# Kernel optimization log

Measured on AMD Instinct MI355X. Metric: run time of the kernel, lower is better.

## Reference

```python
import jax, jax.numpy as jnp
import numpy as np

N, E, F, H, D, O = 100000, 1600000, 128, 128, 64, 1


def setup_inputs() -> dict:
    key = jax.random.key(0)
    ks = jax.random.split(key, 10)
    s = lambda f: np.float32(1.0 / np.sqrt(f))
    return {
        "x": jax.random.normal(ks[0], (N, F), jnp.float32),
        "edge_index": jax.random.randint(ks[1], (2, E), 0, N),
        "W1": jax.random.normal(ks[2], (F, H), jnp.float32) * s(F),
        "b1": jnp.zeros((H,), jnp.float32),
        "Wh": jax.random.normal(ks[3], (H, H), jnp.float32) * s(H),
        "bh": jnp.zeros((H,), jnp.float32),
        "W2": jax.random.normal(ks[4], (H, D), jnp.float32) * s(H),
        "b2": jnp.zeros((D,), jnp.float32),
        "Wo": jax.random.normal(ks[5], (D, O), jnp.float32) * s(D),
        "bo": jnp.zeros((O,), jnp.float32),
    }


def _gcn_layer(h, W, b, src, dst, norm, n):
    # linear transform then normalized sparse aggregation (GCNConv)
    h = h @ W                                   # [n, out]
    msg = h[src] * norm[:, None]                # gather + scale, [E+n, out]
    return jax.ops.segment_sum(msg, dst, num_segments=n) + b


def reference(x, edge_index, W1, b1, Wh, bh, W2, b2, Wo, bo):
    n = x.shape[0]
    loop = jnp.arange(n, dtype=edge_index.dtype)
    src = jnp.concatenate([edge_index[0], loop])  # add self loops
    dst = jnp.concatenate([edge_index[1], loop])
    deg = jax.ops.segment_sum(jnp.ones_like(dst, dtype=x.dtype), dst, num_segments=n)
    dinv = jnp.where(deg > 0, jax.lax.rsqrt(deg), 0.0)
    norm = dinv[src] * dinv[dst]                  # sym-normalized edge weights

    h = jax.nn.relu(_gcn_layer(x, W1, b1, src, dst, norm, n))
    h = jax.nn.relu(_gcn_layer(h, Wh, bh, src, dst, norm, n))
    z = _gcn_layer(h, W2, b2, src, dst, norm, n)  # embedding (no relu after gcn2)
    return z @ Wo + bo                            # node_classification logits [n, 1]
```

## Files before the change

### kernel.cpp

```cpp
#include <hip/hip_runtime.h>
#include <hip/hip_fp16.h>


#define CHUNK 8192
#define ASTR 136

using f16x8 = __attribute__((ext_vector_type(8))) _Float16;
using f32x4 = __attribute__((ext_vector_type(4))) float;

__global__ __launch_bounds__(256) void histH(const int* __restrict__ dst, int* __restrict__ hist,
                                             int E, int NBKT, int NB) {
    __shared__ int bins[1024];
    int blk = blockIdx.x;
    for (int i = threadIdx.x; i < NBKT; i += 256) bins[i] = 0;
    __syncthreads();
    int beg = blk * CHUNK, end = min(E, beg + CHUNK);
    for (int e = beg + threadIdx.x; e < end; e += 256)
        atomicAdd(&bins[dst[e] >> 7], 1);
    __syncthreads();
    for (int i = threadIdx.x; i < NBKT; i += 256)
        hist[i * NB + blk] = bins[i];
}

__global__ __launch_bounds__(256) void scanA(int* __restrict__ hist, int* __restrict__ binsum,
                                             int NBKT, int NB) {
    int wave = (int)((blockIdx.x * (size_t)blockDim.x + threadIdx.x) >> 6);
    if (wave >= NBKT) return;
    int lane = threadIdx.x & 63;
    int* row = hist + (size_t)wave * NB;
    int running = 0;
    for (int b0 = 0; b0 < NB; b0 += 64) {
        int idx = b0 + lane;
        int v = (idx < NB) ? row[idx] : 0;
        int s = v;
#pragma unroll
        for (int off = 1; off < 64; off <<= 1) {
            int u = __shfl_up(s, off, 64);
            if (lane >= off) s += u;
        }
        if (idx < NB) row[idx] = running + s - v;
        running += __shfl(s, 63, 64);
    }
    if (lane == 0) binsum[wave] = running;
}

__global__ void scanK2(const int* __restrict__ binsum, int* __restrict__ binbase,
                       int NBKT, int E) {
    __shared__ int s[1024];
    int t = threadIdx.x;
    int v = (t < NBKT) ? binsum[t] : 0;
    s[t] = v;
    __syncthreads();
    for (int off = 1; off < 1024; off <<= 1) {
        int u = (t >= off) ? s[t - off] : 0;
        __syncthreads();
        s[t] += u;
        __syncthreads();
    }
    if (t < NBKT) binbase[t] = s[t] - v;
    if (t == 0) binbase[NBKT] = E;
}

__global__ __launch_bounds__(256) void scatterH(const int* __restrict__ src,
                                                const int* __restrict__ dst,
                                                const int* __restrict__ hist,
                                                const int* __restrict__ binbase,
                                                int* __restrict__ tmp,
                                                int E, int NBKT, int NB) {
    __shared__ int offs[1024];
    int blk = blockIdx.x;
    for (int i = threadIdx.x; i < NBKT; i += 256)
        offs[i] = hist[i * NB + blk] + binbase[i];
    __syncthreads();
    int beg = blk * CHUNK, end = min(E, beg + CHUNK);
    for (int e = beg + threadIdx.x; e < end; e += 256) {
        int d = dst[e];
        int pos = atomicAdd(&offs[d >> 7], 1);
        tmp[pos] = ((d & 127) << 17) | src[e];
    }
}

__global__ __launch_bounds__(256) void bucket_csr(const int* __restrict__ tmp,
                                                  const int* __restrict__ binbase,
                                                  int* __restrict__ rowptr,
                                                  int* __restrict__ srcidx,
                                                  float* __restrict__ dinv,
                                                  int n) {
    __shared__ int cnt[128], sc[128], cnt2[128];
    int b = blockIdx.x;
    int bstart = binbase[b], bend = binbase[b + 1];
    if (threadIdx.x < 128) cnt[threadIdx.x] = 0;
    __syncthreads();
    for (int e = bstart + threadIdx.x; e < bend; e += 256)
        atomicAdd(&cnt[tmp[e] >> 17], 1);
    __syncthreads();
    if (threadIdx.x < 128) sc[threadIdx.x] = cnt[threadIdx.x];
    __syncthreads();
    for (int off = 1; off < 128; off <<= 1) {
        int u = 0;
        if (threadIdx.x < 128 && threadIdx.x >= off) u = sc[threadIdx.x - off];
        __syncthreads();
        if (threadIdx.x < 128) sc[threadIdx.x] += u;
        __syncthreads();
    }
    if (threadIdx.x < 128) {
        int excl = sc[threadIdx.x] - cnt[threadIdx.x];
        cnt2[threadIdx.x] = excl;
        int id = b * 128 + threadIdx.x;
        if (id <= n) rowptr[id] = bstart + excl;
        if (id < n) dinv[id] = rsqrtf((float)cnt[threadIdx.x] + 1.0f);
    }
    __syncthreads();
    for (int e = bstart + threadIdx.x; e < bend; e += 256) {
        int p = tmp[e];
        int pos = bstart + atomicAdd(&cnt2[p >> 17], 1);
        srcidx[pos] = p & 0x1FFFF;
    }
}

__global__ __launch_bounds__(256) void prep_w(const float* __restrict__ W1,
                                              const float* __restrict__ Wh,
                                              const float* __restrict__ W2,
                                              const float* __restrict__ b2,
                                              const float* __restrict__ Wo,
                                              const float* __restrict__ bo,
                                              __half* __restrict__ Wt1,
                                              __half* __restrict__ WtH,
                                              float* __restrict__ w3,
                                              float* __restrict__ c3) {
    const float* W = blockIdx.x ? Wh : W1;
    __half* Wt = blockIdx.x ? WtH : Wt1;
    for (int i = threadIdx.x; i < 16384; i += 256) {
        int c = i >> 7, k = i & 127;
        Wt[c * 128 + k] = __float2half(W[k * 128 + c]);
    }
    if (blockIdx.x == 0 && threadIdx.x < 128) {
        int j = threadIdx.x;
        float s = 0.f;
        for (int d = 0; d < 64; ++d) s += W2[j * 64 + d] * Wo[d];
        w3[j] = s;
        if (j == 0) {
            float c = 0.f;
            for (int d = 0; d < 64; ++d) c += b2[d] * Wo[d];
            *c3 = c + bo[0];
        }
    }
}

template<typename AT>
__global__ __launch_bounds__(256) void gemm_mfma(const AT* __restrict__ A,
                                                 const __half* __restrict__ Wt,
                                                 const float* __restrict__ dinv,
                                                 __half* __restrict__ Ch, int n) {
    __shared__ _Float16 Al[64 * ASTR];
    __shared__ _Float16 Wl[128 * ASTR];
    const int tid = threadIdx.x;
    const int row0 = blockIdx.x * 64;

#pragma unroll
    for (int i = 0; i < 8; ++i) {
        int idx = tid + 256 * i;
        int c = idx >> 4, q = idx & 15;
        uint4 v = *(const uint4*)(Wt + c * 128 + q * 8);
        *(uint4*)(&Wl[c * ASTR + q * 8]) = v;
    }
#pragma unroll
    for (int i = 0; i < 4; ++i) {
        int idx = tid + 256 * i;
        int r = idx >> 4, q = idx & 15;
        int row = row0 + r;
        uint4 u;
        if constexpr (sizeof(AT) == 2) {
            u = (row < n) ? *(const uint4*)((const __half*)A + (size_t)row * 128 + q * 8)
                          : make_uint4(0u, 0u, 0u, 0u);
        } else {
            if (row < n) {
                const float* ap = (const float*)A + (size_t)row * 128 + q * 8;
                float4 v0 = *(const float4*)ap;
                float4 v1 = *(const float4*)(ap + 4);
                __half2 p0 = __floats2half2_rn(v0.x, v0.y);
                __half2 p1 = __floats2half2_rn(v0.z, v0.w);
                __half2 p2 = __floats2half2_rn(v1.x, v1.y);
                __half2 p3 = __floats2half2_rn(v1.z, v1.w);
                u.x = *(unsigned*)&p0; u.y = *(unsigned*)&p1;
                u.z = *(unsigned*)&p2; u.w = *(unsigned*)&p3;
            } else u = make_uint4(0u, 0u, 0u, 0u);
        }
        *(uint4*)(&Al[r * ASTR + q * 8]) = u;
    }
    __syncthreads();

    const int wave = tid >> 6, lane = tid & 63;
    const int wr = (wave >> 1) * 32;
    const int wc = (wave & 1) * 64;
    const int l = lane & 15, g = lane >> 4;

    f32x4 acc[2][4];
#pragma unroll
    for (int i = 0; i < 2; ++i)
#pragma unroll
        for (int j = 0; j < 4; ++j) acc[i][j] = (f32x4){0.f, 0.f, 0.f, 0.f};

#pragma unroll
    for (int kk = 0; kk < 128; kk += 32) {
        int ko = kk + g * 8;
        f16x8 a0 = *(const f16x8*)(&Al[(wr + l) * ASTR + ko]);
        f16x8 a1 = *(const f16x8*)(&Al[(wr + 16 + l) * ASTR + ko]);
        f16x8 b0 = *(const f16x8*)(&Wl[(wc + l) * ASTR + ko]);
        f16x8 b1 = *(const f16x8*)(&Wl[(wc + 16 + l) * ASTR + ko]);
        f16x8 b2 = *(const f16x8*)(&Wl[(wc + 32 + l) * ASTR + ko]);
        f16x8 b3 = *(const f16x8*)(&Wl[(wc + 48 + l) * ASTR + ko]);
        acc[0][0] = __builtin_amdgcn_mfma_f32_16x16x32_f16(a0, b0, acc[0][0], 0, 0, 0);
        acc[0][1] = __builtin_amdgcn_mfma_f32_16x16x32_f16(a0, b1, acc[0][1], 0, 0, 0);
        acc[0][2] = __builtin_amdgcn_mfma_f32_16x16x32_f16(a0, b2, acc[0][2], 0, 0, 0);
        acc[0][3] = __builtin_amdgcn_mfma_f32_16x16x32_f16(a0, b3, acc[0][3], 0, 0, 0);
        acc[1][0] = __builtin_amdgcn_mfma_f32_16x16x32_f16(a1, b0, acc[1][0], 0, 0, 0);
        acc[1][1] = __builtin_amdgcn_mfma_f32_16x16x32_f16(a1, b1, acc[1][1], 0, 0, 0);
        acc[1][2] = __builtin_amdgcn_mfma_f32_16x16x32_f16(a1, b2, acc[1][2], 0, 0, 0);
        acc[1][3] = __builtin_amdgcn_mfma_f32_16x16x32_f16(a1, b3, acc[1][3], 0, 0, 0);
    }

#pragma unroll
    for (int rt = 0; rt < 2; ++rt) {
#pragma unroll
        for (int j = 0; j < 4; ++j) {
            int row = row0 + wr + rt * 16 + g * 4 + j;
            if (row < n) {
                float di = dinv[row];
#pragma unroll
                for (int ct = 0; ct < 4; ++ct)
                    Ch[(size_t)row * 128 + wc + ct * 16 + l] =
                        __float2half(acc[rt][ct][j] * di);
            }
        }
    }
}

template<int MODE>
__global__ __launch_bounds__(256) void agg_csr(const int* __restrict__ rowptr,
                                               const int* __restrict__ srcidx,
                                               const float* __restrict__ dinv,
                                               const __half* __restrict__ Gh,
                                               const float* __restrict__ bias,
                                               const float* __restrict__ w3,
                                               void* __restrict__ outp, int n) {
    int node = (int)((blockIdx.x * (size_t)blockDim.x + threadIdx.x) >> 5);
    if (node >= n) return;
    const int lane = threadIdx.x & 63;
    const int l32 = lane & 31;
    const int strm = l32 >> 4;
    const int l = l32 & 15;
    const int co = l * 8;
    int beg = rowptr[node], end = rowptr[node + 1];

    float4 aLo = make_float4(0.f, 0.f, 0.f, 0.f);
    float4 aHi = make_float4(0.f, 0.f, 0.f, 0.f);

#define ACC16(u)                                                            \
    {                                                                       \
        float2 f0 = __half22float2(*(const __half2*)&(u).x);                \
        float2 f1 = __half22float2(*(const __half2*)&(u).y);                \
        float2 f2 = __half22float2(*(const __half2*)&(u).z);                \
        float2 f3 = __half22float2(*(const __half2*)&(u).w);                \
        aLo.x += f0.x; aLo.y += f0.y; aLo.z += f1.x; aLo.w += f1.y;         \
        aHi.x += f2.x; aHi.y += f2.y; aHi.z += f3.x; aHi.w += f3.y;         \
    }

    if (strm == 0) {
        uint4 u = *(const uint4*)(Gh + (size_t)node * 128 + co);
        ACC16(u);
    }

    int e = beg + strm;
    for (; e + 6 < end; e += 8) {
        int s0 = srcidx[e], s1 = srcidx[e + 2], s2 = srcidx[e + 4], s3 = srcidx[e + 6];
        const __half* r0 = Gh + (size_t)s0 * 128 + co;
        const __half* r1 = Gh + (size_t)s1 * 128 + co;
        const __half* r2 = Gh + (size_t)s2 * 128 + co;
        const __half* r3 = Gh + (size_t)s3 * 128 + co;
        uint4 u0 = *(const uint4*)r0;
        uint4 u1 = *(const uint4*)r1;
        uint4 u2 = *(const uint4*)r2;
        uint4 u3 = *(const uint4*)r3;
        ACC16(u0);
        ACC16(u1);
        ACC16(u2);
        ACC16(u3);
    }
    for (; e < end; e += 2) {
        int s0 = srcidx[e];
        uint4 u0 = *(const uint4*)(Gh + (size_t)s0 * 128 + co);
        ACC16(u0);
    }
#undef ACC16

    aLo.x += __shfl_xor(aLo.x, 16, 64); aLo.y += __shfl_xor(aLo.y, 16, 64);
    aLo.z += __shfl_xor(aLo.z, 16, 64); aLo.w += __shfl_xor(aLo.w, 16, 64);
    aHi.x += __shfl_xor(aHi.x, 16, 64); aHi.y += __shfl_xor(aHi.y, 16, 64);
    aHi.z += __shfl_xor(aHi.z, 16, 64); aHi.w += __shfl_xor(aHi.w, 16, 64);

    float di = dinv[node];
    float4 b0 = *(const float4*)(bias + co);
    float4 b1 = *(const float4*)(bias + co + 4);
    float o0 = fmaxf(di * aLo.x + b0.x, 0.f);
    float o1 = fmaxf(di * aLo.y + b0.y, 0.f);
    float o2 = fmaxf(di * aLo.z + b0.z, 0.f);
    float o3 = fmaxf(di * aLo.w + b0.w, 0.f);
    float o4 = fmaxf(di * aHi.x + b1.x, 0.f);
    float o5 = fmaxf(di * aHi.y + b1.y, 0.f);
    float o6 = fmaxf(di * aHi.z + b1.z, 0.f);
    float o7 = fmaxf(di * aHi.w + b1.w, 0.f);

    if constexpr (MODE == 0) {
        if (strm == 0) {
            __half2 p0 = __floats2half2_rn(o0, o1);
            __half2 p1 = __floats2half2_rn(o2, o3);
            __half2 p2 = __floats2half2_rn(o4, o5);
            __half2 p3 = __floats2half2_rn(o6, o7);
            uint4 u;
            u.x = *(unsigned*)&p0; u.y = *(unsigned*)&p1;
            u.z = *(unsigned*)&p2; u.w = *(unsigned*)&p3;
            *(uint4*)((__half*)outp + (size_t)node * 128 + co) = u;
        }
    } else {
        float4 w0 = *(const float4*)(w3 + co);
        float4 w1 = *(const float4*)(w3 + co + 4);
        float v = o0 * w0.x + o1 * w0.y + o2 * w0.z + o3 * w0.w
                + o4 * w1.x + o5 * w1.y + o6 * w1.z + o7 * w1.w;
        v += __shfl_xor(v, 1, 64);
        v += __shfl_xor(v, 2, 64);
        v += __shfl_xor(v, 4, 64);
        v += __shfl_xor(v, 8, 64);
        if (l32 == 0) ((float*)outp)[node] = di * v;
    }
}

__global__ void agg_csr_scalar(const int* __restrict__ rowptr, const int* __restrict__ srcidx,
                               const float* __restrict__ dinv, const float* __restrict__ ys,
                               const float* __restrict__ c3, float* __restrict__ out, int n) {
    int i = blockIdx.x * blockDim.x + threadIdx.x;
    if (i >= n) return;
    int beg = rowptr[i], end = rowptr[i + 1];
    float acc = ys[i];
    int e = beg;
    for (; e + 3 < end; e += 4) {
        acc += ys[srcidx[e]] + ys[srcidx[e + 1]] + ys[srcidx[e + 2]] + ys[srcidx[e + 3]];
    }
    for (; e < end; ++e) acc += ys[srcidx[e]];
    out[i] = dinv[i] * acc + c3[0];
}

static inline size_t align4(size_t x) { return (x + 3) & ~(size_t)3; }

extern "C" void kernel_launch(void* const* d_in, const int* in_sizes, int n_in,
                              void* d_out, int out_size, void* d_ws, size_t ws_size,
                              hipStream_t stream) {
    const float* x  = (const float*)d_in[0];
    const int* ei   = (const int*)d_in[1];
    const float* W1 = (const float*)d_in[2];
    const float* b1 = (const float*)d_in[3];
    const float* Wh = (const float*)d_in[4];
    const float* bh = (const float*)d_in[5];
    const float* W2 = (const float*)d_in[6];
    const float* b2 = (const float*)d_in[7];
    const float* Wo = (const float*)d_in[8];
    const float* bo = (const float*)d_in[9];
    float* out = (float*)d_out;

    const int n = in_sizes[0] / 128;
    const int E = in_sizes[1] / 2;
    const int* src = ei;
    const int* dst = ei + E;

    const int NB = (E + CHUNK - 1) / CHUNK;
    const int NBKT = (n >> 7) + 1;

    size_t o = 0;
    int* rowptr = (int*)d_ws + o;        o = align4(o + n + 1);
    int* srcidx = (int*)d_ws + o;        o = align4(o + E);
    int* hist   = (int*)d_ws + o;        o = align4(o + (size_t)NBKT * NB);
    int* binsum = (int*)d_ws + o;        o = align4(o + NBKT);
    int* binbase= (int*)d_ws + o;        o = align4(o + NBKT + 1);
    float* dinv = (float*)d_ws + o;      o = align4(o + n);
    float* w3   = (float*)d_ws + o;      o = align4(o + 128);
    float* c3   = (float*)d_ws + o;      o = align4(o + 4);
    __half* Wt1 = (__half*)((int*)d_ws + o);     o = align4(o + 8192);
    __half* WtH = (__half*)((int*)d_ws + o);     o = align4(o + 8192);
    __half* bufA16 = (__half*)((int*)d_ws + o);  o = align4(o + (size_t)n * 64);
    __half* bufB16 = (__half*)((int*)d_ws + o);  o = align4(o + (size_t)n * 64);
    int* tmp = (int*)bufA16;
    float* ys = (float*)bufB16;

    const int B = (n + 255) / 256;

    histH<<<NB, 256, 0, stream>>>(dst, hist, E, NBKT, NB);
    scanA<<<(NBKT * 64 + 255) / 256, 256, 0, stream>>>(hist, binsum, NBKT, NB);
    scanK2<<<1, 1024, 0, stream>>>(binsum, binbase, NBKT, E);
    scatterH<<<NB, 256, 0, stream>>>(src, dst, hist, binbase, tmp, E, NBKT, NB);
    bucket_csr<<<NBKT, 256, 0, stream>>>(tmp, binbase, rowptr, srcidx, dinv, n);
    prep_w<<<2, 256, 0, stream>>>(W1, Wh, W2, b2, Wo, bo, Wt1, WtH, w3, c3);

    const int GG = (n + 63) / 64;
    const int GA = (int)(((size_t)n * 32 + 255) / 256);

    gemm_mfma<float><<<GG, 256, 0, stream>>>(x, Wt1, dinv, bufA16, n);
    agg_csr<0><<<GA, 256, 0, stream>>>(rowptr, srcidx, dinv, bufA16, b1, w3, bufB16, n);

    gemm_mfma<__half><<<GG, 256, 0, stream>>>(bufB16, WtH, dinv, bufA16, n);
    agg_csr<1><<<GA, 256, 0, stream>>>(rowptr, srcidx, dinv, bufA16, bh, w3, ys, n);

    agg_csr_scalar<<<B, 256, 0, stream>>>(rowptr, srcidx, dinv, ys, c3, out, n);
}
```

Measured before the change: 235.7 us.

## Fuse histogram with first GEMM and move dinv scaling into aggregation

The first GEMM no longer depends on dinv, so it now runs in the same launch as the dst histogram (block index picks the role) and overlaps with CSR construction. Layer‑1 aggregation instead applies dinv[src] per edge, and its output is pre‑scaled by dinv so the second GEMM needs no scaling. bucket_csr caches its bucket's edges in shared memory to avoid rereading tmp, and tmp gets its own workspace buffer because bufA16 is now live during CSR build. The cost is an extra per-edge dinv gather in layer‑1 aggregation and a larger workspace.

```diff
diff --git a/kernel.cpp b/kernel.cpp
--- a/kernel.cpp
+++ b/kernel.cpp
@@ -7,116 +7,6 @@
 
 using f16x8 = __attribute__((ext_vector_type(8))) _Float16;
 using f32x4 = __attribute__((ext_vector_type(4))) float;
-
-__global__ __launch_bounds__(256) void histH(const int* __restrict__ dst, int* __restrict__ hist,
-                                             int E, int NBKT, int NB) {
-    __shared__ int bins[1024];
-    int blk = blockIdx.x;
-    for (int i = threadIdx.x; i < NBKT; i += 256) bins[i] = 0;
-    __syncthreads();
-    int beg = blk * CHUNK, end = min(E, beg + CHUNK);
-    for (int e = beg + threadIdx.x; e < end; e += 256)
-        atomicAdd(&bins[dst[e] >> 7], 1);
-    __syncthreads();
-    for (int i = threadIdx.x; i < NBKT; i += 256)
-        hist[i * NB + blk] = bins[i];
-}
-
-__global__ __launch_bounds__(256) void scanA(int* __restrict__ hist, int* __restrict__ binsum,
-                                             int NBKT, int NB) {
-    int wave = (int)((blockIdx.x * (size_t)blockDim.x + threadIdx.x) >> 6);
-    if (wave >= NBKT) return;
-    int lane = threadIdx.x & 63;
-    int* row = hist + (size_t)wave * NB;
-    int running = 0;
-    for (int b0 = 0; b0 < NB; b0 += 64) {
-        int idx = b0 + lane;
-        int v = (idx < NB) ? row[idx] : 0;
-        int s = v;
-#pragma unroll
-        for (int off = 1; off < 64; off <<= 1) {
-            int u = __shfl_up(s, off, 64);
-            if (lane >= off) s += u;
-        }
-        if (idx < NB) row[idx] = running + s - v;
-        running += __shfl(s, 63, 64);
-    }
-    if (lane == 0) binsum[wave] = running;
-}
-
-__global__ void scanK2(const int* __restrict__ binsum, int* __restrict__ binbase,
-                       int NBKT, int E) {
-    __shared__ int s[1024];
-    int t = threadIdx.x;
-    int v = (t < NBKT) ? binsum[t] : 0;
-    s[t] = v;
-    __syncthreads();
-    for (int off = 1; off < 1024; off <<= 1) {
-        int u = (t >= off) ? s[t - off] : 0;
-        __syncthreads();
-        s[t] += u;
-        __syncthreads();
-    }
-    if (t < NBKT) binbase[t] = s[t] - v;
-    if (t == 0) binbase[NBKT] = E;
-}
-
-__global__ __launch_bounds__(256) void scatterH(const int* __restrict__ src,
-                                                const int* __restrict__ dst,
-                                                const int* __restrict__ hist,
-                                                const int* __restrict__ binbase,
-                                                int* __restrict__ tmp,
-                                                int E, int NBKT, int NB) {
-    __shared__ int offs[1024];
-    int blk = blockIdx.x;
-    for (int i = threadIdx.x; i < NBKT; i += 256)
-        offs[i] = hist[i * NB + blk] + binbase[i];
-    __syncthreads();
-    int beg = blk * CHUNK, end = min(E, beg + CHUNK);
-    for (int e = beg + threadIdx.x; e < end; e += 256) {
-        int d = dst[e];
-        int pos = atomicAdd(&offs[d >> 7], 1);
-        tmp[pos] = ((d & 127) << 17) | src[e];
-    }
-}
-
-__global__ __launch_bounds__(256) void bucket_csr(const int* __restrict__ tmp,
-                                                  const int* __restrict__ binbase,
-                                                  int* __restrict__ rowptr,
-                                                  int* __restrict__ srcidx,
-                                                  float* __restrict__ dinv,
-                                                  int n) {
-    __shared__ int cnt[128], sc[128], cnt2[128];
-    int b = blockIdx.x;
-    int bstart = binbase[b], bend = binbase[b + 1];
-    if (threadIdx.x < 128) cnt[threadIdx.x] = 0;
-    __syncthreads();
-    for (int e = bstart + threadIdx.x; e < bend; e += 256)
-        atomicAdd(&cnt[tmp[e] >> 17], 1);
-    __syncthreads();
-    if (threadIdx.x < 128) sc[threadIdx.x] = cnt[threadIdx.x];
-    __syncthreads();
-    for (int off = 1; off < 128; off <<= 1) {
-        int u = 0;
-        if (threadIdx.x < 128 && threadIdx.x >= off) u = sc[threadIdx.x - off];
-        __syncthreads();
-        if (threadIdx.x < 128) sc[threadIdx.x] += u;
-        __syncthreads();
-    }
-    if (threadIdx.x < 128) {
-        int excl = sc[threadIdx.x] - cnt[threadIdx.x];
-        cnt2[threadIdx.x] = excl;
-        int id = b * 128 + threadIdx.x;
-        if (id <= n) rowptr[id] = bstart + excl;
-        if (id < n) dinv[id] = rsqrtf((float)cnt[threadIdx.x] + 1.0f);
-    }
-    __syncthreads();
-    for (int e = bstart + threadIdx.x; e < bend; e += 256) {
-        int p = tmp[e];
-        int pos = bstart + atomicAdd(&cnt2[p >> 17], 1);
-        srcidx[pos] = p & 0x1FFFF;
-    }
-}
 
 __global__ __launch_bounds__(256) void prep_w(const float* __restrict__ W1,
                                               const float* __restrict__ Wh,
@@ -147,15 +37,28 @@
     }
 }
 
+__device__ __forceinline__ void hist_body(const int* __restrict__ dst,
+                                          int* __restrict__ hist,
+                                          int E, int NBKT, int NB, int blk) {
+    __shared__ int bins[1024];
+    for (int i = threadIdx.x; i < NBKT; i += 256) bins[i] = 0;
+    __syncthreads();
+    int beg = blk * CHUNK, end = min(E, beg + CHUNK);
+    for (int e = beg + threadIdx.x; e < end; e += 256)
+        atomicAdd(&bins[dst[e] >> 7], 1);
+    __syncthreads();
+    for (int i = threadIdx.x; i < NBKT; i += 256)
+        hist[i * NB + blk] = bins[i];
+}
+
 template<typename AT>
-__global__ __launch_bounds__(256) void gemm_mfma(const AT* __restrict__ A,
-                                                 const __half* __restrict__ Wt,
-                                                 const float* __restrict__ dinv,
-                                                 __half* __restrict__ Ch, int n) {
+__device__ __forceinline__ void gemm_body(const AT* __restrict__ A,
+                                          const __half* __restrict__ Wt,
+                                          __half* __restrict__ Ch, int n, int blk) {
     __shared__ _Float16 Al[64 * ASTR];
     __shared__ _Float16 Wl[128 * ASTR];
     const int tid = threadIdx.x;
-    const int row0 = blockIdx.x * 64;
+    const int row0 = blk * 64;
 
 #pragma unroll
     for (int i = 0; i < 8; ++i) {
@@ -226,17 +129,137 @@
         for (int j = 0; j < 4; ++j) {
             int row = row0 + wr + rt * 16 + g * 4 + j;
             if (row < n) {
-                float di = dinv[row];
 #pragma unroll
                 for (int ct = 0; ct < 4; ++ct)
                     Ch[(size_t)row * 128 + wc + ct * 16 + l] =
-                        __float2half(acc[rt][ct][j] * di);
+                        __float2half(acc[rt][ct][j]);
             }
         }
     }
 }
 
-template<int MODE>
+__global__ __launch_bounds__(256) void mega1(const int* __restrict__ dst,
+                                             int* __restrict__ hist,
+                                             int E, int NBKT, int NB,
+                                             const float* __restrict__ x,
+                                             const __half* __restrict__ Wt1,
+                                             __half* __restrict__ g1, int n) {
+    if ((int)blockIdx.x < NB)
+        hist_body(dst, hist, E, NBKT, NB, blockIdx.x);
+    else
+        gemm_body<float>(x, Wt1, g1, n, blockIdx.x - NB);
+}
+
+__global__ __launch_bounds__(256) void gemm2_k(const __half* __restrict__ A,
+                                               const __half* __restrict__ Wt,
+                                               __half* __restrict__ Ch, int n) {
+    gemm_body<__half>(A, Wt, Ch, n, blockIdx.x);
+}
+
+__global__ __launch_bounds__(256) void scanA(int* __restrict__ hist, int* __restrict__ binsum,
+                                             int NBKT, int NB) {
+    int wave = (int)((blockIdx.x * (size_t)blockDim.x + threadIdx.x) >> 6);
+    if (wave >= NBKT) return;
+    int lane = threadIdx.x & 63;
+    int* row = hist + (size_t)wave * NB;
+    int running = 0;
+    for (int b0 = 0; b0 < NB; b0 += 64) {
+        int idx = b0 + lane;
+        int v = (idx < NB) ? row[idx] : 0;
+        int s = v;
+#pragma unroll
+        for (int off = 1; off < 64; off <<= 1) {
+            int u = __shfl_up(s, off, 64);
+            if (lane >= off) s += u;
+        }
+        if (idx < NB) row[idx] = running + s - v;
+        running += __shfl(s, 63, 64);
+    }
+    if (lane == 0) binsum[wave] = running;
+}
+
+__global__ void scanK2(const int* __restrict__ binsum, int* __restrict__ binbase,
+                       int NBKT, int E) {
+    __shared__ int s[1024];
+    int t = threadIdx.x;
+    int v = (t < NBKT) ? binsum[t] : 0;
+    s[t] = v;
+    __syncthreads();
+    for (int off = 1; off < 1024; off <<= 1) {
+        int u = (t >= off) ? s[t - off] : 0;
+        __syncthreads();
+        s[t] += u;
+        __syncthreads();
+    }
+    if (t < NBKT) binbase[t] = s[t] - v;
+    if (t == 0) binbase[NBKT] = E;
+}
+
+__global__ __launch_bounds__(256) void scatterH(const int* __restrict__ src,
+                                                const int* __restrict__ dst,
+                                                const int* __restrict__ hist,
+                                                const int* __restrict__ binbase,
+                                                int* __restrict__ tmp,
+                                                int E, int NBKT, int NB) {
+    __shared__ int offs[1024];
+    int blk = blockIdx.x;
+    for (int i = threadIdx.x; i < NBKT; i += 256)
+        offs[i] = hist[i * NB + blk] + binbase[i];
+    __syncthreads();
+    int beg = blk * CHUNK, end = min(E, beg + CHUNK);
+    for (int e = beg + threadIdx.x; e < end; e += 256) {
+        int d = dst[e];
+        int pos = atomicAdd(&offs[d >> 7], 1);
+        tmp[pos] = ((d & 127) << 17) | src[e];
+    }
+}
+
+#define EBUF 2688
+__global__ __launch_bounds__(256) void bucket_csr(const int* __restrict__ tmp,
+                                                  const int* __restrict__ binbase,
+                                                  int* __restrict__ rowptr,
+                                                  int* __restrict__ srcidx,
+                                                  float* __restrict__ dinv,
+                                                  int n) {
+    __shared__ int cnt[128], sc[128], cnt2[128];
+    __shared__ int ebuf[EBUF];
+    int b = blockIdx.x;
+    int bstart = binbase[b], bend = binbase[b + 1];
+    int cntE = bend - bstart;
+    bool fit = (cntE <= EBUF);
+    if (threadIdx.x < 128) cnt[threadIdx.x] = 0;
+    __syncthreads();
+    for (int e = threadIdx.x; e < cntE; e += 256) {
+        int p = tmp[bstart + e];
+        if (fit) ebuf[e] = p;
+        atomicAdd(&cnt[p >> 17], 1);
+    }
+    __syncthreads();
+    if (threadIdx.x < 128) sc[threadIdx.x] = cnt[threadIdx.x];
+    __syncthreads();
+    for (int off = 1; off < 128; off <<= 1) {
+        int u = 0;
+        if (threadIdx.x < 128 && threadIdx.x >= off) u = sc[threadIdx.x - off];
+        __syncthreads();
+        if (threadIdx.x < 128) sc[threadIdx.x] += u;
+        __syncthreads();
+    }
+    if (threadIdx.x < 128) {
+        int excl = sc[threadIdx.x] - cnt[threadIdx.x];
+        cnt2[threadIdx.x] = excl;
+        int id = b * 128 + threadIdx.x;
+        if (id <= n) rowptr[id] = bstart + excl;
+        if (id < n) dinv[id] = rsqrtf((float)cnt[threadIdx.x] + 1.0f);
+    }
+    __syncthreads();
+    for (int e = threadIdx.x; e < cntE; e += 256) {
+        int p = fit ? ebuf[e] : tmp[bstart + e];
+        int pos = bstart + atomicAdd(&cnt2[p >> 17], 1);
+        srcidx[pos] = p & 0x1FFFF;
+    }
+}
+
+template<int MODE, int EDGE_DINV>
 __global__ __launch_bounds__(256) void agg_csr(const int* __restrict__ rowptr,
                                                const int* __restrict__ srcidx,
                                                const float* __restrict__ dinv,
@@ -252,54 +275,56 @@
     const int l = l32 & 15;
     const int co = l * 8;
     int beg = rowptr[node], end = rowptr[node + 1];
+    float di = dinv[node];
 
     float4 aLo = make_float4(0.f, 0.f, 0.f, 0.f);
     float4 aHi = make_float4(0.f, 0.f, 0.f, 0.f);
 
-#define ACC16(u)                                                            \
+#define ACCS(u, s)                                                          \
     {                                                                       \
         float2 f0 = __half22float2(*(const __half2*)&(u).x);                \
         float2 f1 = __half22float2(*(const __half2*)&(u).y);                \
         float2 f2 = __half22float2(*(const __half2*)&(u).z);                \
         float2 f3 = __half22float2(*(const __half2*)&(u).w);                \
-        aLo.x += f0.x; aLo.y += f0.y; aLo.z += f1.x; aLo.w += f1.y;         \
-        aHi.x += f2.x; aHi.y += f2.y; aHi.z += f3.x; aHi.w += f3.y;         \
+        aLo.x = fmaf(f0.x, s, aLo.x); aLo.y = fmaf(f0.y, s, aLo.y);         \
+        aLo.z = fmaf(f1.x, s, aLo.z); aLo.w = fmaf(f1.y, s, aLo.w);         \
+        aHi.x = fmaf(f2.x, s, aHi.x); aHi.y = fmaf(f2.y, s, aHi.y);         \
+        aHi.z = fmaf(f3.x, s, aHi.z); aHi.w = fmaf(f3.y, s, aHi.w);         \
     }
 
     if (strm == 0) {
         uint4 u = *(const uint4*)(Gh + (size_t)node * 128 + co);
-        ACC16(u);
+        float sf = EDGE_DINV ? di : 1.0f;
+        ACCS(u, sf);
     }
 
     int e = beg + strm;
     for (; e + 6 < end; e += 8) {
         int s0 = srcidx[e], s1 = srcidx[e + 2], s2 = srcidx[e + 4], s3 = srcidx[e + 6];
-        const __half* r0 = Gh + (size_t)s0 * 128 + co;
-        const __half* r1 = Gh + (size_t)s1 * 128 + co;
-        const __half* r2 = Gh + (size_t)s2 * 128 + co;
-        const __half* r3 = Gh + (size_t)s3 * 128 + co;
-        uint4 u0 = *(const uint4*)r0;
-        uint4 u1 = *(const uint4*)r1;
-        uint4 u2 = *(const uint4*)r2;
-        uint4 u3 = *(const uint4*)r3;
-        ACC16(u0);
-        ACC16(u1);
-        ACC16(u2);
-        ACC16(u3);
+        float d0 = 1.f, d1 = 1.f, d2 = 1.f, d3 = 1.f;
+        if (EDGE_DINV) { d0 = dinv[s0]; d1 = dinv[s1]; d2 = dinv[s2]; d3 = dinv[s3]; }
+        uint4 u0 = *(const uint4*)(Gh + (size_t)s0 * 128 + co);
+        uint4 u1 = *(const uint4*)(Gh + (size_t)s1 * 128 + co);
+        uint4 u2 = *(const uint4*)(Gh + (size_t)s2 * 128 + co);
+        uint4 u3 = *(const uint4*)(Gh + (size_t)s3 * 128 + co);
+        ACCS(u0, d0);
+        ACCS(u1, d1);
+        ACCS(u2, d2);
+        ACCS(u3, d3);
     }
     for (; e < end; e += 2) {
         int s0 = srcidx[e];
+        float d0 = EDGE_DINV ? dinv[s0] : 1.0f;
         uint4 u0 = *(const uint4*)(Gh + (size_t)s0 * 128 + co);
-        ACC16(u0);
-    }
-#undef ACC16
+        ACCS(u0, d0);
+    }
+#undef ACCS
 
     aLo.x += __shfl_xor(aLo.x, 16, 64); aLo.y += __shfl_xor(aLo.y, 16, 64);
     aLo.z += __shfl_xor(aLo.z, 16, 64); aLo.w += __shfl_xor(aLo.w, 16, 64);
     aHi.x += __shfl_xor(aHi.x, 16, 64); aHi.y += __shfl_xor(aHi.y, 16, 64);
     aHi.z += __shfl_xor(aHi.z, 16, 64); aHi.w += __shfl_xor(aHi.w, 16, 64);
 
-    float di = dinv[node];
     float4 b0 = *(const float4*)(bias + co);
     float4 b1 = *(const float4*)(bias + co + 4);
     float o0 = fmaxf(di * aLo.x + b0.x, 0.f);
@@ -313,10 +338,10 @@
 
     if constexpr (MODE == 0) {
         if (strm == 0) {
-            __half2 p0 = __floats2half2_rn(o0, o1);
-            __half2 p1 = __floats2half2_rn(o2, o3);
-            __half2 p2 = __floats2half2_rn(o4, o5);
-            __half2 p3 = __floats2half2_rn(o6, o7);
+            __half2 p0 = __floats2half2_rn(di * o0, di * o1);
+            __half2 p1 = __floats2half2_rn(di * o2, di * o3);
+            __half2 p2 = __floats2half2_rn(di * o4, di * o5);
+            __half2 p3 = __floats2half2_rn(di * o6, di * o7);
             uint4 u;
             u.x = *(unsigned*)&p0; u.y = *(unsigned*)&p1;
             u.z = *(unsigned*)&p2; u.w = *(unsigned*)&p3;
@@ -378,6 +403,7 @@
     size_t o = 0;
     int* rowptr = (int*)d_ws + o;        o = align4(o + n + 1);
     int* srcidx = (int*)d_ws + o;        o = align4(o + E);
+    int* tmp    = (int*)d_ws + o;        o = align4(o + E);
     int* hist   = (int*)d_ws + o;        o = align4(o + (size_t)NBKT * NB);
     int* binsum = (int*)d_ws + o;        o = align4(o + NBKT);
     int* binbase= (int*)d_ws + o;        o = align4(o + NBKT + 1);
@@ -388,26 +414,25 @@
     __half* WtH = (__half*)((int*)d_ws + o);     o = align4(o + 8192);
     __half* bufA16 = (__half*)((int*)d_ws + o);  o = align4(o + (size_t)n * 64);
     __half* bufB16 = (__half*)((int*)d_ws + o);  o = align4(o + (size_t)n * 64);
-    int* tmp = (int*)bufA16;
     float* ys = (float*)bufB16;
 
     const int B = (n + 255) / 256;
-
-    histH<<<NB, 256, 0, stream>>>(dst, hist, E, NBKT, NB);
+    const int GG = (n + 63) / 64;
+    const int GA = (int)(((size_t)n * 32 + 255) / 256);
+
+    prep_w<<<2, 256, 0, stream>>>(W1, Wh, W2, b2, Wo, bo, Wt1, WtH, w3, c3);
+
+    mega1<<<NB + GG, 256, 0, stream>>>(dst, hist, E, NBKT, NB, x, Wt1, bufA16, n);
+
     scanA<<<(NBKT * 64 + 255) / 256, 256, 0, stream>>>(hist, binsum, NBKT, NB);
     scanK2<<<1, 1024, 0, stream>>>(binsum, binbase, NBKT, E);
     scatterH<<<NB, 256, 0, stream>>>(src, dst, hist, binbase, tmp, E, NBKT, NB);
     bucket_csr<<<NBKT, 256, 0, stream>>>(tmp, binbase, rowptr, srcidx, dinv, n);
-    prep_w<<<2, 256, 0, stream>>>(W1, Wh, W2, b2, Wo, bo, Wt1, WtH, w3, c3);
-
-    const int GG = (n + 63) / 64;
-    const int GA = (int)(((size_t)n * 32 + 255) / 256);
-
-    gemm_mfma<float><<<GG, 256, 0, stream>>>(x, Wt1, dinv, bufA16, n);
-    agg_csr<0><<<GA, 256, 0, stream>>>(rowptr, srcidx, dinv, bufA16, b1, w3, bufB16, n);
-
-    gemm_mfma<__half><<<GG, 256, 0, stream>>>(bufB16, WtH, dinv, bufA16, n);
-    agg_csr<1><<<GA, 256, 0, stream>>>(rowptr, srcidx, dinv, bufA16, bh, w3, ys, n);
+
+    agg_csr<0, 1><<<GA, 256, 0, stream>>>(rowptr, srcidx, dinv, bufA16, b1, w3, bufB16, n);
+
+    gemm2_k<<<GG, 256, 0, stream>>>(bufB16, WtH, bufA16, n);
+    agg_csr<1, 0><<<GA, 256, 0, stream>>>(rowptr, srcidx, dinv, bufA16, bh, w3, ys, n);
 
     agg_csr_scalar<<<B, 256, 0, stream>>>(rowptr, srcidx, dinv, ys, c3, out, n);
 }
```

New measurement: 222.4 us. 5.6% less time.
